# Optimization experiments

Measured on AMD Instinct MI355X. Metric: run time of the kernel, lower is better.

## Reference

```python
import jax, jax.numpy as jnp
import numpy as np

N = 10000          # nodes
E = 160000         # directed edges (before self loops)
H = 6              # GATConv heads (hardcoded in init_conv)
D = 128            # in_channels = hidden = out_channels
L = 4              # len(hidden_dims) + 1 conv layers
NEG_SLOPE = 0.2    # GATConv default leaky_relu slope


def setup_inputs() -> dict:
    key = jax.random.key(0)
    ks = jax.random.split(key, 2 + 4 * L)
    inp = {}
    inp["x"] = jax.random.normal(ks[0], (N, D), dtype=jnp.float32)
    inp["edge_index"] = jax.random.randint(ks[1], (2, E), 0, N, dtype=jnp.int64)
    for i in range(L):
        kW, ka, kb, kbias = jax.random.split(ks[2 + i], 4)
        scale = 1.0 / np.sqrt(D)
        inp[f"W{i}"] = jax.random.normal(kW, (D, H * D), dtype=jnp.float32) * scale
        inp[f"att_src{i}"] = jax.random.normal(ka, (1, H, D), dtype=jnp.float32) * scale
        inp[f"att_dst{i}"] = jax.random.normal(kb, (1, H, D), dtype=jnp.float32) * scale
        inp[f"b{i}"] = jnp.zeros((D,), dtype=jnp.float32)
    return inp


def _gat_layer(x, src, dst, W, att_src, att_dst, bias):
    # x: [N, Din]; src/dst: [E'] (with self loops); W: [Din, H*C]
    n = x.shape[0]
    xw = (x @ W).reshape(n, H, -1)                      # [N, H, C]
    a_src = jnp.sum(xw * att_src, axis=-1)              # [N, H]
    a_dst = jnp.sum(xw * att_dst, axis=-1)              # [N, H]
    e = jax.nn.leaky_relu(a_src[src] + a_dst[dst], NEG_SLOPE)  # [E', H]
    # segment softmax over edges grouped by destination node
    m = jax.lax.stop_gradient(jax.ops.segment_max(e, dst, num_segments=n))
    e = jnp.exp(e - m[dst])
    denom = jax.ops.segment_sum(e, dst, num_segments=n)  # [N, H]
    alpha = e / (denom[dst] + 1e-16)                     # [E', H]
    out = jax.ops.segment_sum(alpha[:, :, None] * xw[src], dst, num_segments=n)  # [N, H, C]
    return jnp.mean(out, axis=1) + bias                  # concat=False -> head mean


def reference(x, edge_index,
              W0, att_src0, att_dst0, b0,
              W1, att_src1, att_dst1, b1,
              W2, att_src2, att_dst2, b2,
              W3, att_src3, att_dst3, b3):
    n = x.shape[0]
    loops = jnp.arange(n, dtype=edge_index.dtype)
    src = jnp.concatenate([edge_index[0], loops])  # add_self_loops=True
    dst = jnp.concatenate([edge_index[1], loops])
    params = [(W0, att_src0, att_dst0, b0), (W1, att_src1, att_dst1, b1),
              (W2, att_src2, att_dst2, b2), (W3, att_src3, att_dst3, b3)]
    for (W, a_s, a_d, b) in params:
        x = _gat_layer(x, src, dst, W, a_s, a_d, b)
        x = jax.nn.relu(x)  # norm=Identity, dropout eval/no-op; relu applied every layer (jk_mode set)
    return x
```

## Files before the change

kernel.cpp:

```cpp
#include <hip/hip_runtime.h>
#include <hip/hip_fp16.h>
#include <math.h>

#define H 6
#define D 128
#define K_ALL (H * D)
#define TSTEPS 24
#define PADK 776
#define NPB 8

typedef _Float16 f16x8 __attribute__((ext_vector_type(8)));
typedef float f32x4 __attribute__((ext_vector_type(4)));

struct FoldArgs {
    const float* W[4];
    const float* as[4];
    const float* ad[4];
};


__global__ __launch_bounds__(256) void zero_kernel(int4* __restrict__ p, int n4) {
    int i = blockIdx.x * 256 + threadIdx.x;
    if (i < n4) p[i] = make_int4(0, 0, 0, 0);
}

__global__ __launch_bounds__(256) void hist_prep1_kernel(const int* __restrict__ dst,
                                                         int* __restrict__ deg, int E,
                                                         int histBlocks, FoldArgs fa,
                                                         float* __restrict__ wa_all) {
    int b = blockIdx.x;
    int tid = threadIdx.x;
    if (b < histBlocks) {
        int e = b * 256 + tid;
        if (e < E) atomicAdd(&deg[dst[e]], 1);
    } else {
        int t = (b - histBlocks) * 256 + tid;
        if (t >= 4 * 1536) return;
        int l = t / 1536;
        int r = t % 1536;
        int k = r / 12, j = r % 12;
        int h = (j < 6) ? j : (j - 6);
        const float* att = (j < 6) ? fa.as[l] : fa.ad[l];
        const float* wrow = fa.W[l] + (size_t)k * K_ALL + h * D;
        const float* arow = att + h * D;
        float s = 0.f;
        #pragma unroll 8
        for (int c = 0; c < D; c++) s += wrow[c] * arow[c];
        wa_all[(size_t)l * 1536 + k * 12 + j] = s;
    }
}

__global__ __launch_bounds__(1024) void scan_kernel(const int* __restrict__ deg,
                                                    int* __restrict__ rowptr, int n,
                                                    const float* __restrict__ wa_all,
                                                    _Float16* __restrict__ waf) {
    __shared__ int wsum[16];
    const int tid = threadIdx.x;
    const int lane = tid & 63;
    const int wv = tid >> 6;
    const int base = tid << 4;

    int v[16];
    int tot = 0;
    #pragma unroll
    for (int k = 0; k < 16; k++) {
        int i = base + k;
        int d = (i < n) ? deg[i] : 0;
        v[k] = tot;
        tot += d;
    }
    int s = tot;
    #pragma unroll
    for (int off = 1; off < 64; off <<= 1) {
        int t = __shfl_up(s, off, 64);
        if (lane >= off) s += t;
    }
    if (lane == 63) wsum[wv] = s;
    __syncthreads();
    if (tid < 16) {
        int t = wsum[tid];
        #pragma unroll
        for (int off = 1; off < 16; off <<= 1) {
            int u = __shfl_up(t, off, 64);
            if ((int)tid >= off) t += u;
        }
        wsum[tid] = t;
    }
    __syncthreads();
    int off0 = ((wv > 0) ? wsum[wv - 1] : 0) + s - tot;
    #pragma unroll
    for (int k = 0; k < 16; k++) {
        int i = base + k;
        if (i < n) rowptr[i] = off0 + v[k];
    }

    {
        int L = tid >> 8;
        int t = (tid >> 6) & 3;
        int j = lane & 15;
        const float* wl = wa_all + (size_t)L * 1536;
        f16x8 vv;
        #pragma unroll
        for (int jj = 0; jj < 8; jj++) {
            int k = t * 32 + ((lane >> 4) << 3) + jj;
            float sv = (j < 12) ? wl[k * 12 + j] : 0.f;
            vv[jj] = (_Float16)sv;
        }
        *(f16x8*)(waf + (size_t)L * 2048 + (size_t)t * 512 + (size_t)lane * 8) = vv;
    }
}

__global__ __launch_bounds__(256) void scatter_prep2_kernel(const int* __restrict__ src,
                                                            const int* __restrict__ dst,
                                                            int* __restrict__ rowcur,
                                                            int* __restrict__ col, int E,
                                                            int scatBlocks, FoldArgs fa,
                                                            const _Float16* __restrict__ waf,
                                                            _Float16* __restrict__ bf,
                                                            const float* __restrict__ x_in,
                                                            float* __restrict__ a0, int N) {
    __shared__ _Float16 xs[16][136];
    int b = blockIdx.x;
    int tid = threadIdx.x;
    if (b < scatBlocks) {
        int e = b * 256 + tid;
        if (e < E) {
            int p = atomicAdd(&rowcur[dst[e]], 1);
            col[p] = src[e];
        }
        return;
    }
    int bb = b - scatBlocks;
    if (bb < 192) {
        int idx = bb * 256 + tid;
        int l63 = idx & 63;
        int ct = (idx >> 6) & 7;
        int t = (idx >> 9) % TSTEPS;
        int layer = idx / (TSTEPS * 8 * 64);
        const float* W = fa.W[layer];
        int c = ct * 16 + (l63 & 15);
        f16x8 v;
        #pragma unroll
        for (int j = 0; j < 8; j++) {
            int k = t * 32 + ((l63 >> 4) << 3) + j;
            v[j] = (_Float16)W[(size_t)(k & 127) * K_ALL + ((k >> 7) << 7) + c];
        }
        *(f16x8*)(bf + ((size_t)idx << 3)) = v;
        return;
    }
    bb -= 192;
    int base_node = bb << 4;
    {
        int row = tid >> 4;
        int coff = (tid & 15) * 8;
        int node = base_node + row;
        f16x8 v = {};
        if (node < N) {
            const float* sp = x_in + (size_t)node * D + coff;
            float4 u0 = *(const float4*)sp;
            float4 u1 = *(const float4*)(sp + 4);
            v[0] = (_Float16)u0.x; v[1] = (_Float16)u0.y;
            v[2] = (_Float16)u0.z; v[3] = (_Float16)u0.w;
            v[4] = (_Float16)u1.x; v[5] = (_Float16)u1.y;
            v[6] = (_Float16)u1.z; v[7] = (_Float16)u1.w;
        }
        *(f16x8*)&xs[row][coff] = v;
    }
    __syncthreads();
    if (tid < 64) {
        int lane = tid;
        int cl = lane & 15;
        int r0 = (lane >> 4) << 2;
        f32x4 ac = {0.f, 0.f, 0.f, 0.f};
        #pragma unroll
        for (int t = 0; t < 4; t++) {
            f16x8 av = *(const f16x8*)&xs[cl][t * 32 + ((lane >> 4) << 3)];
            f16x8 bv = *(const f16x8*)(waf + (size_t)t * 512 + (size_t)lane * 8);
            ac = __builtin_amdgcn_mfma_f32_16x16x32_f16(av, bv, ac, 0, 0, 0);
        }
        if (cl < 12) {
            #pragma unroll
            for (int reg = 0; reg < 4; reg++) {
                int node = base_node + r0 + reg;
                if (node < N) a0[(size_t)node * 12 + cl] = ac[reg];
            }
        }
    }
}

__device__ __forceinline__ float rlf(float v, int j) {
    return __int_as_float(__builtin_amdgcn_readlane(__float_as_int(v), j));
}

__device__ __forceinline__ void aggregate_node(const float* __restrict__ x,
                                               const float* __restrict__ a,
                                               const int* __restrict__ rowend,
                                               const int* __restrict__ deg_,
                                               const int* __restrict__ col,
                                               int n, int lane,
                                               _Float16* __restrict__ xsrow) {
    const int deg = deg_[n];
    const int start = rowend[n] - deg;
    const int nent = deg + 1;

    float adst[H];
    #pragma unroll
    for (int h = 0; h < H; h++) adst[h] = a[(size_t)n * 12 + 6 + h];

    if (nent <= 64) {
        int s = n;
        if (lane < deg) s = col[start + lane];

        const float* as_ = a + (size_t)s * 12;
        float4 v0 = *(const float4*)as_;
        float2 v1 = *(const float2*)(as_ + 4);
        float e0 = v0.x + adst[0], e1 = v0.y + adst[1], e2 = v0.z + adst[2];
        float e3 = v0.w + adst[3], e4 = v1.x + adst[4], e5 = v1.y + adst[5];
        e0 = e0 > 0.f ? e0 : 0.2f * e0;  e1 = e1 > 0.f ? e1 : 0.2f * e1;
        e2 = e2 > 0.f ? e2 : 0.2f * e2;  e3 = e3 > 0.f ? e3 : 0.2f * e3;
        e4 = e4 > 0.f ? e4 : 0.2f * e4;  e5 = e5 > 0.f ? e5 : 0.2f * e5;
        float w0 = __expf(e0), w1 = __expf(e1), w2 = __expf(e2);
        float w3 = __expf(e3), w4 = __expf(e4), w5 = __expf(e5);

        float d0 = 0, d1 = 0, d2 = 0, d3 = 0, d4 = 0, d5 = 0;
        float a00 = 0, a01 = 0, a02 = 0, a03 = 0, a04 = 0, a05 = 0;
        float a10 = 0, a11 = 0, a12 = 0, a13 = 0, a14 = 0, a15 = 0;
        const float* xb = x + (lane << 1);

        float2 xa, xbv;
        {
            int s0 = __builtin_amdgcn_readlane(s, 0);
            xa = *(const float2*)(xb + (size_t)s0 * D);
        }
        xbv = make_float2(0.f, 0.f);
        if (nent > 1) {
            int s1 = __builtin_amdgcn_readlane(s, 1);
            xbv = *(const float2*)(xb + (size_t)s1 * D);
        }
        for (int j = 0; j < nent; j += 2) {
            float2 xn0 = make_float2(0.f, 0.f), xn1 = make_float2(0.f, 0.f);
            if (j + 2 < nent) {
                int s2 = __builtin_amdgcn_readlane(s, j + 2);
                xn0 = *(const float2*)(xb + (size_t)s2 * D);
            }
            if (j + 3 < nent) {
                int s3 = __builtin_amdgcn_readlane(s, j + 3);
                xn1 = *(const float2*)(xb + (size_t)s3 * D);
            }
            {
                float b0 = rlf(w0, j), b1 = rlf(w1, j), b2 = rlf(w2, j);
                float b3 = rlf(w3, j), b4 = rlf(w4, j), b5 = rlf(w5, j);
                d0 += b0; d1 += b1; d2 += b2; d3 += b3; d4 += b4; d5 += b5;
                a00 += b0 * xa.x; a10 += b0 * xa.y;
                a01 += b1 * xa.x; a11 += b1 * xa.y;
                a02 += b2 * xa.x; a12 += b2 * xa.y;
                a03 += b3 * xa.x; a13 += b3 * xa.y;
                a04 += b4 * xa.x; a14 += b4 * xa.y;
                a05 += b5 * xa.x; a15 += b5 * xa.y;
            }
            if (j + 1 < nent) {
                float b0 = rlf(w0, j + 1), b1 = rlf(w1, j + 1), b2 = rlf(w2, j + 1);
                float b3 = rlf(w3, j + 1), b4 = rlf(w4, j + 1), b5 = rlf(w5, j + 1);
                d0 += b0; d1 += b1; d2 += b2; d3 += b3; d4 += b4; d5 += b5;
                a00 += b0 * xbv.x; a10 += b0 * xbv.y;
                a01 += b1 * xbv.x; a11 += b1 * xbv.y;
                a02 += b2 * xbv.x; a12 += b2 * xbv.y;
                a03 += b3 * xbv.x; a13 += b3 * xbv.y;
                a04 += b4 * xbv.x; a14 += b4 * xbv.y;
                a05 += b5 * xbv.x; a15 += b5 * xbv.y;
            }
            xa = xn0; xbv = xn1;
        }
        float i0 = 1.f / d0, i1 = 1.f / d1, i2 = 1.f / d2;
        float i3 = 1.f / d3, i4 = 1.f / d4, i5 = 1.f / d5;
        int c = lane << 1;
        xsrow[0 * D + c] = (_Float16)(a00 * i0);  xsrow[0 * D + c + 1] = (_Float16)(a10 * i0);
        xsrow[1 * D + c] = (_Float16)(a01 * i1);  xsrow[1 * D + c + 1] = (_Float16)(a11 * i1);
        xsrow[2 * D + c] = (_Float16)(a02 * i2);  xsrow[2 * D + c + 1] = (_Float16)(a12 * i2);
        xsrow[3 * D + c] = (_Float16)(a03 * i3);  xsrow[3 * D + c + 1] = (_Float16)(a13 * i3);
        xsrow[4 * D + c] = (_Float16)(a04 * i4);  xsrow[4 * D + c + 1] = (_Float16)(a14 * i4);
        xsrow[5 * D + c] = (_Float16)(a05 * i5);  xsrow[5 * D + c + 1] = (_Float16)(a15 * i5);
    } else {
        float d[H] = {0, 0, 0, 0, 0, 0};
        float acc0[H] = {0, 0, 0, 0, 0, 0};
        float acc1[H] = {0, 0, 0, 0, 0, 0};
        int c0 = lane, c1 = 64 + lane;
        for (int j = 0; j <= deg; j++) {
            int s = (j < deg) ? col[start + j] : n;
            float w[H];
            #pragma unroll
            for (int h = 0; h < H; h++) {
                float e = a[(size_t)s * 12 + h] + adst[h];
                e = (e > 0.f) ? e : 0.2f * e;
                w[h] = __expf(e);
                d[h] += w[h];
            }
            float xv0 = x[(size_t)s * D + c0];
            float xv1 = x[(size_t)s * D + c1];
            #pragma unroll
            for (int h = 0; h < H; h++) {
                acc0[h] += w[h] * xv0;
                acc1[h] += w[h] * xv1;
            }
        }
        #pragma unroll
        for (int h = 0; h < H; h++) {
            float inv = 1.0f / d[h];
            xsrow[h * D + c0] = (_Float16)(acc0[h] * inv);
            xsrow[h * D + c1] = (_Float16)(acc1[h] * inv);
        }
    }
}

__global__ __launch_bounds__(512) void layer_kernel(const float* __restrict__ x,
                                                    const float* __restrict__ a_in,
                                                    const int* __restrict__ rowend,
                                                    const int* __restrict__ deg_,
                                                    const int* __restrict__ col,
                                                    const _Float16* __restrict__ bf,
                                                    const float* __restrict__ bias,
                                                    float* __restrict__ xout,
                                                    const _Float16* __restrict__ awf,
                                                    float* __restrict__ a_out, int M) {
    __shared__ _Float16 xs16[16][PADK];
    __shared__ _Float16 xso[16][136];
    const int wave = (int)(threadIdx.x >> 6);
    const int lane = (int)(threadIdx.x & 63);
    const int m0 = (int)(blockIdx.x << 3);

    {
        int n = m0 + wave;
        if (n < M)
            aggregate_node(x, a_in, rowend, deg_, col, n, lane, &xs16[wave][0]);
    }
    __syncthreads();

    f32x4 acc = {0.f, 0.f, 0.f, 0.f};
    const _Float16* ars = &xs16[lane & 15][(lane >> 4) << 3];
    const _Float16* bp = bf + (size_t)wave * 512 + (size_t)lane * 8;
    for (int t = 0; t < TSTEPS; t++) {
        f16x8 av = *(const f16x8*)(ars + t * 32);
        f16x8 bv = *(const f16x8*)(bp + (size_t)t * 4096);
        acc = __builtin_amdgcn_mfma_f32_16x16x32_f16(av, bv, acc, 0, 0, 0);
    }

    const float inv6 = 1.0f / 6.0f;
    const int cl = lane & 15;
    const int ccol = wave * 16 + cl;
    const int r0 = (lane >> 4) << 2;
    const float bs = bias[ccol];
    #pragma unroll
    for (int reg = 0; reg < 4; reg++) {
        int ml = r0 + reg;
        int m = m0 + ml;
        float v = acc[reg] * inv6 + bs;
        v = v > 0.f ? v : 0.f;
        if (ml < NPB && m < M) xout[(size_t)m * D + ccol] = v;
        xso[ml][ccol] = (_Float16)v;
    }

    if (awf) {
        __syncthreads();
        if (wave == 0) {
            f32x4 ac = {0.f, 0.f, 0.f, 0.f};
            #pragma unroll
            for (int t = 0; t < 4; t++) {
                f16x8 av = *(const f16x8*)&xso[cl][t * 32 + ((lane >> 4) << 3)];
                f16x8 bv = *(const f16x8*)(awf + (size_t)t * 512 + (size_t)lane * 8);
                ac = __builtin_amdgcn_mfma_f32_16x16x32_f16(av, bv, ac, 0, 0, 0);
            }
            if (cl < 12) {
                #pragma unroll
                for (int reg = 0; reg < 4; reg++) {
                    int ml = r0 + reg;
                    int m = m0 + ml;
                    if (ml < NPB && m < M) a_out[(size_t)m * 12 + cl] = ac[reg];
                }
            }
        }
    }
}


extern "C" void kernel_launch(void* const* d_in, const int* in_sizes, int n_in,
                              void* d_out, int out_size, void* d_ws, size_t ws_size,
                              hipStream_t stream) {
    const float* x_in = (const float*)d_in[0];
    const int* ei = (const int*)d_in[1];
    int N = in_sizes[0] / D;
    int E = in_sizes[1] / 2;
    const int* srcp = ei;
    const int* dstp = ei + E;

    size_t bf_halves_per_layer = (size_t)TSTEPS * 8 * 512;

    float* ws = (float*)d_ws;
    float* bufA = ws;
    float* bufB = bufA + (size_t)N * D;
    float* abuf0 = bufB + (size_t)N * D;
    float* abuf1 = abuf0 + (size_t)N * 12;
    float* wa_all = abuf1 + (size_t)N * 12;
    _Float16* waf = (_Float16*)(wa_all + 4 * 1536);
    _Float16* w16f = waf + 4 * 2048;
    int* deg = (int*)(w16f + 4 * bf_halves_per_layer);
    int* rowptr = deg + N;
    int* col = rowptr + (N + 1);

    FoldArgs fa;
    for (int l = 0; l < 4; l++) {
        fa.W[l]  = (const float*)d_in[2 + 4 * l];
        fa.as[l] = (const float*)d_in[3 + 4 * l];
        fa.ad[l] = (const float*)d_in[4 + 4 * l];
    }

    int n4 = (N + 3) / 4;
    zero_kernel<<<(n4 + 255) / 256, 256, 0, stream>>>((int4*)deg, n4);
    int histBlocks = (E + 255) / 256;
    hist_prep1_kernel<<<histBlocks + 24, 256, 0, stream>>>(dstp, deg, E, histBlocks, fa, wa_all);
    scan_kernel<<<1, 1024, 0, stream>>>(deg, rowptr, N, wa_all, waf);
    int scatBlocks = (E + 255) / 256;
    int a0Blocks = (N + 15) / 16;
    scatter_prep2_kernel<<<scatBlocks + 192 + a0Blocks, 256, 0, stream>>>(
        srcp, dstp, rowptr, col, E, scatBlocks, fa, waf, w16f, x_in, abuf0, N);

    const float* xcur = x_in;
    float* acur = abuf0;
    float* anext = abuf1;
    for (int l = 0; l < 4; l++) {
        const float* b = (const float*)d_in[5 + 4 * l];
        float* xout = (l == 3) ? (float*)d_out : ((l & 1) ? bufB : bufA);
        const _Float16* awf = (l < 3) ? (waf + (size_t)(l + 1) * 2048) : (const _Float16*)nullptr;

        layer_kernel<<<(N + NPB - 1) / NPB, 512, 0, stream>>>(xcur, acur, rowptr, deg, col,
                                                              w16f + (size_t)l * bf_halves_per_layer,
                                                              b, xout, awf, anext, N);
        xcur = xout;
        float* tmp = acur; acur = anext; anext = tmp;
    }
}
```

Before: 163.0 us.

## Replace CSR build with fixed-stride per-node bucket adjacency, drop scan kernel

```diff
diff --git a/kernel.cpp b/kernel.cpp
--- a/kernel.cpp
+++ b/kernel.cpp
@@ -8,6 +8,7 @@
 #define TSTEPS 24
 #define PADK 776
 #define NPB 8
+#define BSTRIDE 128
 
 typedef _Float16 f16x8 __attribute__((ext_vector_type(8)));
 typedef float f32x4 __attribute__((ext_vector_type(4)));
@@ -19,114 +20,51 @@
 };
 
 
-__global__ __launch_bounds__(256) void zero_kernel(int4* __restrict__ p, int n4) {
-    int i = blockIdx.x * 256 + threadIdx.x;
-    if (i < n4) p[i] = make_int4(0, 0, 0, 0);
-}
-
-__global__ __launch_bounds__(256) void hist_prep1_kernel(const int* __restrict__ dst,
-                                                         int* __restrict__ deg, int E,
-                                                         int histBlocks, FoldArgs fa,
-                                                         float* __restrict__ wa_all) {
+__global__ __launch_bounds__(256) void zero_wa_kernel(int4* __restrict__ degz, int n4,
+                                                      int zBlocks, FoldArgs fa,
+                                                      float* __restrict__ wa_all) {
     int b = blockIdx.x;
     int tid = threadIdx.x;
-    if (b < histBlocks) {
-        int e = b * 256 + tid;
-        if (e < E) atomicAdd(&deg[dst[e]], 1);
-    } else {
-        int t = (b - histBlocks) * 256 + tid;
-        if (t >= 4 * 1536) return;
-        int l = t / 1536;
-        int r = t % 1536;
-        int k = r / 12, j = r % 12;
-        int h = (j < 6) ? j : (j - 6);
-        const float* att = (j < 6) ? fa.as[l] : fa.ad[l];
-        const float* wrow = fa.W[l] + (size_t)k * K_ALL + h * D;
-        const float* arow = att + h * D;
-        float s = 0.f;
-        #pragma unroll 8
-        for (int c = 0; c < D; c++) s += wrow[c] * arow[c];
-        wa_all[(size_t)l * 1536 + k * 12 + j] = s;
-    }
-}
-
-__global__ __launch_bounds__(1024) void scan_kernel(const int* __restrict__ deg,
-                                                    int* __restrict__ rowptr, int n,
+    if (b < zBlocks) {
+        int i = b * 256 + tid;
+        if (i < n4) degz[i] = make_int4(0, 0, 0, 0);
+        return;
+    }
+    int t = (b - zBlocks) * 256 + tid;
+    if (t >= 4 * 1536) return;
+    int l = t / 1536;
+    int r = t % 1536;
+    int k = r / 12, j = r % 12;
+    int h = (j < 6) ? j : (j - 6);
+    const float* att = (j < 6) ? fa.as[l] : fa.ad[l];
+    const float* wrow = fa.W[l] + (size_t)k * K_ALL + h * D;
+    const float* arow = att + h * D;
+    float s = 0.f;
+    #pragma unroll 8
+    for (int c = 0; c < D; c++) s += wrow[c] * arow[c];
+    wa_all[(size_t)l * 1536 + k * 12 + j] = s;
+}
+
+
+__global__ __launch_bounds__(256) void prep2_kernel(const int* __restrict__ src,
+                                                    const int* __restrict__ dst,
+                                                    int* __restrict__ deg,
+                                                    int* __restrict__ col, int E,
+                                                    int scatBlocks, FoldArgs fa,
                                                     const float* __restrict__ wa_all,
-                                                    _Float16* __restrict__ waf) {
-    __shared__ int wsum[16];
-    const int tid = threadIdx.x;
-    const int lane = tid & 63;
-    const int wv = tid >> 6;
-    const int base = tid << 4;
-
-    int v[16];
-    int tot = 0;
-    #pragma unroll
-    for (int k = 0; k < 16; k++) {
-        int i = base + k;
-        int d = (i < n) ? deg[i] : 0;
-        v[k] = tot;
-        tot += d;
-    }
-    int s = tot;
-    #pragma unroll
-    for (int off = 1; off < 64; off <<= 1) {
-        int t = __shfl_up(s, off, 64);
-        if (lane >= off) s += t;
-    }
-    if (lane == 63) wsum[wv] = s;
-    __syncthreads();
-    if (tid < 16) {
-        int t = wsum[tid];
-        #pragma unroll
-        for (int off = 1; off < 16; off <<= 1) {
-            int u = __shfl_up(t, off, 64);
-            if ((int)tid >= off) t += u;
-        }
-        wsum[tid] = t;
-    }
-    __syncthreads();
-    int off0 = ((wv > 0) ? wsum[wv - 1] : 0) + s - tot;
-    #pragma unroll
-    for (int k = 0; k < 16; k++) {
-        int i = base + k;
-        if (i < n) rowptr[i] = off0 + v[k];
-    }
-
-    {
-        int L = tid >> 8;
-        int t = (tid >> 6) & 3;
-        int j = lane & 15;
-        const float* wl = wa_all + (size_t)L * 1536;
-        f16x8 vv;
-        #pragma unroll
-        for (int jj = 0; jj < 8; jj++) {
-            int k = t * 32 + ((lane >> 4) << 3) + jj;
-            float sv = (j < 12) ? wl[k * 12 + j] : 0.f;
-            vv[jj] = (_Float16)sv;
-        }
-        *(f16x8*)(waf + (size_t)L * 2048 + (size_t)t * 512 + (size_t)lane * 8) = vv;
-    }
-}
-
-__global__ __launch_bounds__(256) void scatter_prep2_kernel(const int* __restrict__ src,
-                                                            const int* __restrict__ dst,
-                                                            int* __restrict__ rowcur,
-                                                            int* __restrict__ col, int E,
-                                                            int scatBlocks, FoldArgs fa,
-                                                            const _Float16* __restrict__ waf,
-                                                            _Float16* __restrict__ bf,
-                                                            const float* __restrict__ x_in,
-                                                            float* __restrict__ a0, int N) {
+                                                    _Float16* __restrict__ waf,
+                                                    _Float16* __restrict__ bf,
+                                                    const float* __restrict__ x_in,
+                                                    float* __restrict__ a0, int N) {
     __shared__ _Float16 xs[16][136];
     int b = blockIdx.x;
     int tid = threadIdx.x;
     if (b < scatBlocks) {
         int e = b * 256 + tid;
         if (e < E) {
-            int p = atomicAdd(&rowcur[dst[e]], 1);
-            col[p] = src[e];
+            int n = dst[e];
+            int p = atomicAdd(&deg[n], 1);
+            if (p < BSTRIDE) col[(size_t)n * BSTRIDE + p] = src[e];
         }
         return;
     }
@@ -149,6 +87,23 @@
         return;
     }
     bb -= 192;
+    if (bb < 4) {
+        int L = bb;
+        int lane = tid & 63;
+        int t = tid >> 6;
+        int j = lane & 15;
+        const float* wl = wa_all + (size_t)L * 1536;
+        f16x8 vv;
+        #pragma unroll
+        for (int jj = 0; jj < 8; jj++) {
+            int k = t * 32 + ((lane >> 4) << 3) + jj;
+            float sv = (j < 12) ? wl[k * 12 + j] : 0.f;
+            vv[jj] = (_Float16)sv;
+        }
+        *(f16x8*)(waf + (size_t)L * 2048 + (size_t)t * 512 + (size_t)lane * 8) = vv;
+        return;
+    }
+    bb -= 4;
     int base_node = bb << 4;
     {
         int row = tid >> 4;
@@ -171,11 +126,18 @@
         int lane = tid;
         int cl = lane & 15;
         int r0 = (lane >> 4) << 2;
+        const float* wl0 = wa_all;
         f32x4 ac = {0.f, 0.f, 0.f, 0.f};
         #pragma unroll
         for (int t = 0; t < 4; t++) {
             f16x8 av = *(const f16x8*)&xs[cl][t * 32 + ((lane >> 4) << 3)];
-            f16x8 bv = *(const f16x8*)(waf + (size_t)t * 512 + (size_t)lane * 8);
+            f16x8 bv;
+            #pragma unroll
+            for (int jj = 0; jj < 8; jj++) {
+                int k = t * 32 + ((lane >> 4) << 3) + jj;
+                float sv = (cl < 12) ? wl0[k * 12 + cl] : 0.f;
+                bv[jj] = (_Float16)sv;
+            }
             ac = __builtin_amdgcn_mfma_f32_16x16x32_f16(av, bv, ac, 0, 0, 0);
         }
         if (cl < 12) {
@@ -194,13 +156,12 @@
 
 __device__ __forceinline__ void aggregate_node(const float* __restrict__ x,
                                                const float* __restrict__ a,
-                                               const int* __restrict__ rowend,
                                                const int* __restrict__ deg_,
                                                const int* __restrict__ col,
                                                int n, int lane,
                                                _Float16* __restrict__ xsrow) {
     const int deg = deg_[n];
-    const int start = rowend[n] - deg;
+    const int start = n << 7;
     const int nent = deg + 1;
 
     float adst[H];
@@ -281,12 +242,13 @@
         xsrow[4 * D + c] = (_Float16)(a04 * i4);  xsrow[4 * D + c + 1] = (_Float16)(a14 * i4);
         xsrow[5 * D + c] = (_Float16)(a05 * i5);  xsrow[5 * D + c + 1] = (_Float16)(a15 * i5);
     } else {
+        int dl = deg < BSTRIDE ? deg : BSTRIDE;
         float d[H] = {0, 0, 0, 0, 0, 0};
         float acc0[H] = {0, 0, 0, 0, 0, 0};
         float acc1[H] = {0, 0, 0, 0, 0, 0};
         int c0 = lane, c1 = 64 + lane;
-        for (int j = 0; j <= deg; j++) {
-            int s = (j < deg) ? col[start + j] : n;
+        for (int j = 0; j <= dl; j++) {
+            int s = (j < dl) ? col[start + j] : n;
             float w[H];
             #pragma unroll
             for (int h = 0; h < H; h++) {
@@ -314,7 +276,6 @@
 
 __global__ __launch_bounds__(512) void layer_kernel(const float* __restrict__ x,
                                                     const float* __restrict__ a_in,
-                                                    const int* __restrict__ rowend,
                                                     const int* __restrict__ deg_,
                                                     const int* __restrict__ col,
                                                     const _Float16* __restrict__ bf,
@@ -331,7 +292,7 @@
     {
         int n = m0 + wave;
         if (n < M)
-            aggregate_node(x, a_in, rowend, deg_, col, n, lane, &xs16[wave][0]);
+            aggregate_node(x, a_in, deg_, col, n, lane, &xs16[wave][0]);
     }
     __syncthreads();
 
@@ -403,8 +364,7 @@
     _Float16* waf = (_Float16*)(wa_all + 4 * 1536);
     _Float16* w16f = waf + 4 * 2048;
     int* deg = (int*)(w16f + 4 * bf_halves_per_layer);
-    int* rowptr = deg + N;
-    int* col = rowptr + (N + 1);
+    int* col = deg + N;
 
     FoldArgs fa;
     for (int l = 0; l < 4; l++) {
@@ -414,14 +374,13 @@
     }
 
     int n4 = (N + 3) / 4;
-    zero_kernel<<<(n4 + 255) / 256, 256, 0, stream>>>((int4*)deg, n4);
-    int histBlocks = (E + 255) / 256;
-    hist_prep1_kernel<<<histBlocks + 24, 256, 0, stream>>>(dstp, deg, E, histBlocks, fa, wa_all);
-    scan_kernel<<<1, 1024, 0, stream>>>(deg, rowptr, N, wa_all, waf);
+    int zBlocks = (n4 + 255) / 256;
+    zero_wa_kernel<<<zBlocks + 24, 256, 0, stream>>>((int4*)deg, n4, zBlocks, fa, wa_all);
+
     int scatBlocks = (E + 255) / 256;
     int a0Blocks = (N + 15) / 16;
-    scatter_prep2_kernel<<<scatBlocks + 192 + a0Blocks, 256, 0, stream>>>(
-        srcp, dstp, rowptr, col, E, scatBlocks, fa, waf, w16f, x_in, abuf0, N);
+    prep2_kernel<<<scatBlocks + 192 + 4 + a0Blocks, 256, 0, stream>>>(
+        srcp, dstp, deg, col, E, scatBlocks, fa, wa_all, waf, w16f, x_in, abuf0, N);
 
     const float* xcur = x_in;
     float* acur = abuf0;
@@ -431,7 +390,7 @@
         float* xout = (l == 3) ? (float*)d_out : ((l & 1) ? bufB : bufA);
         const _Float16* awf = (l < 3) ? (waf + (size_t)(l + 1) * 2048) : (const _Float16*)nullptr;
 
-        layer_kernel<<<(N + NPB - 1) / NPB, 512, 0, stream>>>(xcur, acur, rowptr, deg, col,
+        layer_kernel<<<(N + NPB - 1) / NPB, 512, 0, stream>>>(xcur, acur, deg, col,
                                                               w16f + (size_t)l * bf_halves_per_layer,
                                                               b, xout, awf, anext, N);
         xcur = xout;
```

Measured after the change: 140.4 us. -13.8%, faster.
